# Kernel tuning notes

Measured on AMD Instinct MI355X. Metric: run time of the kernel, lower is better.

The kernel has to match this reference:

```python
import jax, jax.numpy as jnp
import numpy as np

N_ATOMS = 20000        # nodes
N_EDGES = 400000       # avg degree 20
C = 4                  # num_pseudo_species channels
F_IN = 128             # ps_input_size
CONV = [64, 64]        # conv_sizes
HID = [64, 32]         # hidden_sizes
OUT = 1                # output_size (energy)
N_STRUCT = 32          # structures in batch
AVG_ATOMS = 20.0       # average_number_of_atoms
NEG_SLOPE = 0.2        # GAT leaky_relu slope


def setup_inputs() -> dict:
    key = jax.random.key(0)
    ks = jax.random.split(key, 16)
    x = jax.random.normal(ks[0], (N_ATOMS, C, F_IN), dtype=jnp.float32)
    edge_index = jax.random.randint(ks[1], (2, N_EDGES), 0, N_ATOMS)
    batch_ids = jnp.sort(jax.random.randint(ks[2], (N_ATOMS,), 0, N_STRUCT))

    def w(k, shape, fan_in):
        return jax.random.normal(k, shape, dtype=jnp.float32) / np.float32(np.sqrt(fan_in))

    return {
        "x": x,
        "edge_index": edge_index,
        "batch_ids": batch_ids,
        "gamma": jnp.ones((F_IN,), jnp.float32),
        "beta": jnp.zeros((F_IN,), jnp.float32),
        # MultiChannelGATConv 1: F_IN -> 64
        "Wc1": w(ks[3], (C, F_IN, CONV[0]), F_IN),
        "asrc1": w(ks[4], (C, CONV[0]), CONV[0]),
        "adst1": w(ks[5], (C, CONV[0]), CONV[0]),
        # MultiChannelGATConv 2: 64 -> 64
        "Wc2": w(ks[6], (C, CONV[0], CONV[1]), CONV[0]),
        "asrc2": w(ks[7], (C, CONV[1]), CONV[1]),
        "adst2": w(ks[8], (C, CONV[1]), CONV[1]),
        # MultiChannelLinear MLP: 64 -> 64 -> 32
        "Wn1": w(ks[9], (C, CONV[1], HID[0]), CONV[1]),
        "Wn2": w(ks[10], (C, HID[0], HID[1]), HID[0]),
        # out_linear: 32 -> 1
        "Wout": w(ks[11], (C, HID[1], OUT), HID[1]),
    }


def _layer_norm(x, gamma, beta):
    mu = jnp.mean(x, axis=-1, keepdims=True)
    var = jnp.mean((x - mu) ** 2, axis=-1, keepdims=True)
    return (x - mu) * jax.lax.rsqrt(var + 1e-5) * gamma + beta


def _gat_conv(x, W, a_src, a_dst, src, dst):
    # per-channel GATConv (single head, no bias): x [N,C,Fin] -> [N,C,Fout]
    h = jnp.einsum('ncf,cfo->nco', x, W)                       # [N,C,Fout]
    e_src = jnp.einsum('nco,co->nc', h, a_src)                 # [N,C]
    e_dst = jnp.einsum('nco,co->nc', h, a_dst)                 # [N,C]
    logit = jax.nn.leaky_relu(e_src[src] + e_dst[dst], NEG_SLOPE)  # [E,C]
    m = jax.ops.segment_max(logit, dst, num_segments=N_ATOMS)      # [N,C]
    ex = jnp.exp(logit - m[dst])                                   # [E,C]
    den = jax.ops.segment_sum(ex, dst, num_segments=N_ATOMS)       # [N,C]
    alpha = ex / (den[dst] + 1e-16)                                # [E,C]
    msg = alpha[:, :, None] * h[src]                               # [E,C,Fout]
    return jax.ops.segment_sum(msg, dst, num_segments=N_ATOMS)     # [N,C,Fout]


def reference(x, edge_index, batch_ids, gamma, beta,
              Wc1, asrc1, adst1, Wc2, asrc2, adst2,
              Wn1, Wn2, Wout):
    src, dst = edge_index[0], edge_index[1]
    h = _layer_norm(x, gamma, beta)
    h = jax.nn.silu(_gat_conv(h, Wc1, asrc1, adst1, src, dst))
    h = jax.nn.silu(_gat_conv(h, Wc2, asrc2, adst2, src, dst))
    h = jax.nn.silu(jnp.einsum('ncf,cfo->nco', h, Wn1))
    h = jax.nn.silu(jnp.einsum('ncf,cfo->nco', h, Wn2))
    h = jnp.einsum('ncf,cfo->nco', h, Wout)                    # [N,C,1]
    feats = jnp.sum(h, axis=1)                                  # sum_over_components -> [N,1]
    energies = jax.ops.segment_sum(feats, batch_ids, num_segments=N_STRUCT)  # [S,1]
    energies = energies / jnp.sqrt(jnp.float32(C))
    energies = energies / jnp.float32(AVG_ATOMS)
    return energies
```

## Files before the change

### kernel.cpp

```cpp
#include <hip/hip_runtime.h>
#include <hip/hip_bf16.h>
#include <hip/hip_fp16.h>

#define N_ATOMS 20000
#define N_EDGES 400000
#define NCH 4
#define F_IN 128
#define S_OUT 32

__device__ __forceinline__ float silu_f(float v) { return v / (1.f + __expf(-v)); }

typedef _Float16 half8v __attribute__((ext_vector_type(8)));
typedef float f32x4v __attribute__((ext_vector_type(4)));

__device__ __forceinline__ half8v ld_frag(const __half* p) {
    union { float4 f; half8v h; } u;
    u.f = *(const float4*)p;
    return u.h;
}

__device__ __forceinline__ int wave_iscan(int v, int l) {
#pragma unroll
    for (int off = 1; off < 64; off <<= 1) {
        int t = __shfl_up(v, off);
        if (l >= off) v += t;
    }
    return v;
}

__global__ void fill_kernel(float* __restrict__ p, int n, float v) {
    int i = blockIdx.x * blockDim.x + threadIdx.x;
    int stride = gridDim.x * blockDim.x;
    for (; i < n; i += stride) p[i] = v;
}

__global__ void hist_kernel(const int* __restrict__ ei, int* __restrict__ cnt, int E) {
    int e = blockIdx.x * 256 + threadIdx.x;
    if (e < E) atomicAdd(&cnt[ei[E + e]], 1);
}

__global__ __launch_bounds__(256) void scan_l1_kernel(const int* __restrict__ cnt,
                                                      int* __restrict__ rowp,
                                                      int* __restrict__ bsum, int n) {
    int i = blockIdx.x * 256 + threadIdx.x;
    int l = threadIdx.x & 63, w = threadIdx.x >> 6;
    int v = (i < n) ? cnt[i] : 0;
    int incl = wave_iscan(v, l);
    __shared__ int wsum[4];
    if (l == 63) wsum[w] = incl;
    __syncthreads();
    int add = 0;
#pragma unroll
    for (int j = 0; j < 4; ++j) add += (j < w) ? wsum[j] : 0;
    if (i < n) rowp[i] = add + incl - v;
    if (threadIdx.x == 255) bsum[blockIdx.x] = add + incl;
}

__global__ __launch_bounds__(256) void scan_l2_kernel(const int* __restrict__ bsum,
                                                      int* __restrict__ boff,
                                                      int* __restrict__ rowp_n, int nb,
                                                      float* __restrict__ out_zero) {
    int i = threadIdx.x;
    if (i < S_OUT) out_zero[i] = 0.f;
    int l = i & 63, w = i >> 6;
    int v = (i < nb) ? bsum[i] : 0;
    int incl = wave_iscan(v, l);
    __shared__ int wsum[4];
    if (l == 63) wsum[w] = incl;
    __syncthreads();
    int add = 0;
#pragma unroll
    for (int j = 0; j < 4; ++j) add += (j < w) ? wsum[j] : 0;
    if (i < nb) boff[i] = add + incl - v;
    if (i == nb - 1) *rowp_n = add + incl;
}

__global__ __launch_bounds__(256) void scan_l3_kernel(int* __restrict__ rowp,
                                                      const int* __restrict__ boff, int n) {
    int i = blockIdx.x * 256 + threadIdx.x;
    if (i < n) rowp[i] += boff[blockIdx.x];
}

__global__ void scatter_kernel(const int* __restrict__ ei, const int* __restrict__ rowp,
                               int* __restrict__ fill, int* __restrict__ csr_src, int E) {
    int e = blockIdx.x * 256 + threadIdx.x;
    if (e < E) {
        int d = ei[E + e];
        int pos = rowp[d] + atomicAdd(&fill[d], 1);
        csr_src[pos] = ei[e];
    }
}

template <int FIN, int IN_STRIDE, bool IN_HALF, bool IN_CMAJ, bool LN, bool ATT,
          bool SILU_OUT, bool OUT_HALF, bool OUT_CMAJ>
__global__ __launch_bounds__(256) void proj_kernel(const void* __restrict__ inv,
                                                   const float* __restrict__ gamma,
                                                   const float* __restrict__ beta,
                                                   const float* __restrict__ W,
                                                   const float* __restrict__ a_src,
                                                   const float* __restrict__ a_dst,
                                                   void* __restrict__ outv,
                                                   float* __restrict__ es,
                                                   float* __restrict__ ed) {
    constexpr int OCT = FIN / 8;
    constexpr int OM = OCT - 1;
    constexpr int WSH = FIN + 8;
    __shared__ __half Wt[64 * WSH];
    __shared__ __half inl[64 * WSH];
    const int tid = threadIdx.x;
    const int c = blockIdx.y;
    const int n0 = blockIdx.x * 64;
    const int w = tid >> 6;
    const int l = tid & 63;
    const int col = l & 15;
    const int g = l >> 4;

    const float* __restrict__ Wc = W + c * (FIN * 64);
    for (int i = tid; i < (FIN / 2) * 64; i += 256) {
        int kp = i >> 6, oo = i & 63;
        int k = kp * 2;
        float w0 = Wc[(size_t)k * 64 + oo];
        float w1 = Wc[(size_t)(k + 1) * 64 + oo];
        int pos = ((((k >> 3) ^ (oo >> 2)) & OM) << 3) | (k & 7);
        *(__half2*)(&Wt[oo * WSH + pos]) = __floats2half2_rn(w0, w1);
    }
    if (IN_HALF) {
        const __half* __restrict__ inh = (const __half*)inv;
        for (int i = tid; i < 64 * (FIN / 8); i += 256) {
            int nl = i / (FIN / 8), ch = i % (FIN / 8);
            int node = min(n0 + nl, N_ATOMS - 1);
            const __half* src = IN_CMAJ
                ? inh + ((size_t)c * N_ATOMS + node) * 64 + ch * 8
                : inh + (size_t)node * IN_STRIDE + c * FIN + ch * 8;
            *(float4*)(inl + nl * WSH + ch * 8) = *(const float4*)src;
        }
    } else {
        const float* __restrict__ inf = (const float*)inv;
        for (int i = tid; i < 64 * (FIN / 8); i += 256) {
            int nl = i / (FIN / 8), ch = i % (FIN / 8);
            int node = min(n0 + nl, N_ATOMS - 1);
            const float* src = inf + (size_t)node * IN_STRIDE + c * FIN + ch * 8;
            float4 a = *(const float4*)src;
            float4 b = *(const float4*)(src + 4);
            float4 st;
            __half2* sp = (__half2*)&st;
            sp[0] = __floats2half2_rn(a.x, a.y);
            sp[1] = __floats2half2_rn(a.z, a.w);
            sp[2] = __floats2half2_rn(b.x, b.y);
            sp[3] = __floats2half2_rn(b.z, b.w);
            *(float4*)(inl + nl * WSH + ch * 8) = st;
        }
    }
    __syncthreads();

    if (LN) {
        int sub = l >> 4;
        int l16 = l & 15;
        float gv[8], bv8[8];
#pragma unroll
        for (int j = 0; j < 8; ++j) {
            gv[j] = gamma[l16 * 8 + j];
            bv8[j] = beta[l16 * 8 + j];
        }
#pragma unroll
        for (int it = 0; it < 4; ++it) {
            int row = w * 16 + it * 4 + sub;
            __half* rp = inl + row * WSH + l16 * 8;
            float4 raw = *(const float4*)rp;
            __half2* hp = (__half2*)&raw;
            float v[8];
#pragma unroll
            for (int j = 0; j < 4; ++j) {
                float2 f = __half22float2(hp[j]);
                v[2 * j] = f.x;
                v[2 * j + 1] = f.y;
            }
            float s = 0.f, sq = 0.f;
#pragma unroll
            for (int j = 0; j < 8; ++j) { s += v[j]; sq += v[j] * v[j]; }
#pragma unroll
            for (int off = 1; off < 16; off <<= 1) {
                s += __shfl_xor(s, off);
                sq += __shfl_xor(sq, off);
            }
            float mu = s * (1.f / 128.f);
            float rs = rsqrtf(sq * (1.f / 128.f) - mu * mu + 1e-5f);
            float4 st;
            __half2* sp = (__half2*)&st;
#pragma unroll
            for (int j = 0; j < 4; ++j)
                sp[j] = __floats2half2_rn((v[2 * j] - mu) * rs * gv[2 * j] + bv8[2 * j],
                                          (v[2 * j + 1] - mu) * rs * gv[2 * j + 1] + bv8[2 * j + 1]);
            *(float4*)rp = st;
        }
        __syncthreads();
    }

    f32x4v acc[4];
#pragma unroll
    for (int t = 0; t < 4; ++t) acc[t] = (f32x4v){0.f, 0.f, 0.f, 0.f};

    const __half* arow = inl + (w * 16 + col) * WSH + g * 8;
#pragma unroll
    for (int it = 0; it < FIN / 32; ++it) {
        half8v af = ld_frag(arow + it * 32);
        int J = it * 4 + g;
#pragma unroll
        for (int t = 0; t < 4; ++t) {
            int oo = 16 * t + col;
            half8v bf = ld_frag(Wt + oo * WSH + (((J ^ (oo >> 2)) & OM) << 3));
            acc[t] = __builtin_amdgcn_mfma_f32_16x16x32_f16(af, bf, acc[t], 0, 0, 0);
        }
    }

    float av[4], bv[4];
    if (ATT) {
#pragma unroll
        for (int t = 0; t < 4; ++t) {
            av[t] = a_src[c * 64 + 16 * t + col];
            bv[t] = a_dst[c * 64 + 16 * t + col];
        }
    }
#pragma unroll
    for (int r = 0; r < 4; ++r) {
        int node = n0 + w * 16 + g * 4 + r;
        bool valid = node < N_ATOMS;
        if (valid) {
#pragma unroll
            for (int t = 0; t < 4; ++t) {
                float o = acc[t][r];
                if (SILU_OUT) o = silu_f(o);
                size_t idx = OUT_CMAJ ? ((size_t)c * N_ATOMS + node) * 64 + 16 * t + col
                                      : (size_t)node * 256 + c * 64 + 16 * t + col;
                if (OUT_HALF)
                    ((__half*)outv)[idx] = __float2half(o);
                else
                    ((float*)outv)[idx] = o;
            }
        }
        if (ATT) {
            float ps = 0.f, pd = 0.f;
#pragma unroll
            for (int t = 0; t < 4; ++t) {
                ps = fmaf(acc[t][r], av[t], ps);
                pd = fmaf(acc[t][r], bv[t], pd);
            }
#pragma unroll
            for (int off = 1; off < 16; off <<= 1) {
                ps += __shfl_xor(ps, off);
                pd += __shfl_xor(pd, off);
            }
            if (col == 0 && valid) { es[node * NCH + c] = ps; ed[node * NCH + c] = pd; }
        }
    }
}

__global__ __launch_bounds__(256) void gat_gather_kernel(const int* __restrict__ rowp,
                                                         const int* __restrict__ csr_src,
                                                         const float* __restrict__ es,
                                                         const float* __restrict__ ed,
                                                         const __half* __restrict__ h,
                                                         __half* __restrict__ out) {
    int l = threadIdx.x & 63;
    int d = blockIdx.x * 4 + (threadIdx.x >> 6);
    int c = blockIdx.y;
    int q = l & 15;
    int g = l >> 4;
    int grp = l & 48;
    const __half* __restrict__ hc = h + (size_t)c * N_ATOMS * 64;
    int r0 = rowp[d], r1 = rowp[d + 1];
    float edc = ed[d * NCH + c];
    float m = -1e30f, den = 0.f;
    float a0 = 0.f, a1 = 0.f, a2 = 0.f, a3 = 0.f;

    for (int base = r0; base < r1; base += 16) {
        int len = min(16, r1 - base);
        float logit = -1e30f;
        int s = 0;
        if (q < len) {
            s = csr_src[base + q];
            float v = es[s * NCH + c] + edc;
            logit = v >= 0.f ? v : 0.2f * v;
        }
        float cm = logit;
#pragma unroll
        for (int off = 8; off; off >>= 1) cm = fmaxf(cm, __shfl_xor(cm, off));
        float nm = fmaxf(m, cm);
        float resc = __expf(m - nm);
        float ex = (q < len) ? __expf(logit - nm) : 0.f;
        float cs = ex;
#pragma unroll
        for (int off = 8; off; off >>= 1) cs += __shfl_xor(cs, off);
        den = den * resc + cs;
        a0 *= resc; a1 *= resc; a2 *= resc; a3 *= resc;
        m = nm;
#pragma unroll
        for (int j = 0; j < 4; ++j) {
            int e = g + 4 * j;
            bool act = e < len;
            int ee = act ? e : 0;
            float xe = __shfl(ex, grp | ee);
            int se = __shfl(s, grp | ee);
            xe = act ? xe : 0.f;
            float2 hv = *(const float2*)(hc + (size_t)se * 64 + q * 4);
            __half2* hp = (__half2*)&hv;
            float2 f0 = __half22float2(hp[0]), f1 = __half22float2(hp[1]);
            a0 = fmaf(xe, f0.x, a0);
            a1 = fmaf(xe, f0.y, a1);
            a2 = fmaf(xe, f1.x, a2);
            a3 = fmaf(xe, f1.y, a3);
        }
    }
#pragma unroll
    for (int off = 16; off < 64; off <<= 1) {
        a0 += __shfl_xor(a0, off);
        a1 += __shfl_xor(a1, off);
        a2 += __shfl_xor(a2, off);
        a3 += __shfl_xor(a3, off);
    }
    if (g == 0) {
        float inv = 1.f / (den + 1e-16f);
        float2 st;
        __half2* sp = (__half2*)&st;
        sp[0] = __floats2half2_rn(silu_f(a0 * inv), silu_f(a1 * inv));
        sp[1] = __floats2half2_rn(silu_f(a2 * inv), silu_f(a3 * inv));
        *(float2*)(out + ((size_t)c * N_ATOMS + d) * 64 + q * 4) = st;
    }
}

__global__ __launch_bounds__(256) void mlp_fused_kernel(const __half* __restrict__ in,
                                                        const float* __restrict__ W1,
                                                        const float* __restrict__ W2,
                                                        const float* __restrict__ W3,
                                                        const int* __restrict__ bat,
                                                        float* __restrict__ out) {
    constexpr int WSH = 72;
    __shared__ __half W1t[64 * WSH];
    __shared__ __half inl[64 * WSH];
    __shared__ __half t1l[64 * WSH];
    __shared__ __half W2t[NCH][32 * WSH];
    __shared__ float w3l[NCH * 32];
    __shared__ float ynode[64];
    const int tid = threadIdx.x;
    const int n0 = blockIdx.x * 64;
    const int w = tid >> 6;
    const int l = tid & 63;
    const int col = l & 15;
    const int g = l >> 4;

    for (int i = tid; i < NCH * 32 * 32; i += 256) {
        int cc = i >> 10, rem = i & 1023;
        int kp = rem >> 5, o2 = rem & 31;
        int k = kp * 2;
        float a = W2[cc * 2048 + k * 32 + o2];
        float b = W2[cc * 2048 + (k + 1) * 32 + o2];
        int pos = ((((k >> 3) ^ (o2 >> 2)) & 7) << 3) | (k & 7);
        *(__half2*)(&W2t[cc][o2 * WSH + pos]) = __floats2half2_rn(a, b);
    }
    if (tid < NCH * 32) w3l[tid] = W3[tid];

    float yacc[4] = {0.f, 0.f, 0.f, 0.f};

    for (int c = 0; c < NCH; ++c) {
        __syncthreads();
        for (int i = tid; i < 32 * 64; i += 256) {
            int kp = i >> 6, oo = i & 63;
            int k = kp * 2;
            float a = W1[c * 4096 + k * 64 + oo];
            float b = W1[c * 4096 + (k + 1) * 64 + oo];
            int pos = ((((k >> 3) ^ (oo >> 2)) & 7) << 3) | (k & 7);
            *(__half2*)(&W1t[oo * WSH + pos]) = __floats2half2_rn(a, b);
        }
        for (int i = tid; i < 64 * 8; i += 256) {
            int nl = i >> 3, ch = i & 7;
            int node = min(n0 + nl, N_ATOMS - 1);
            *(float4*)(inl + nl * WSH + ch * 8) =
                *(const float4*)(in + ((size_t)c * N_ATOMS + node) * 64 + ch * 8);
        }
        __syncthreads();

        f32x4v acc[4];
#pragma unroll
        for (int t = 0; t < 4; ++t) acc[t] = (f32x4v){0.f, 0.f, 0.f, 0.f};
        const __half* arow = inl + (w * 16 + col) * WSH + g * 8;
#pragma unroll
        for (int it = 0; it < 2; ++it) {
            half8v af = ld_frag(arow + it * 32);
            int J = it * 4 + g;
#pragma unroll
            for (int t = 0; t < 4; ++t) {
                int oo = 16 * t + col;
                half8v bf = ld_frag(W1t + oo * WSH + (((J ^ (oo >> 2)) & 7) << 3));
                acc[t] = __builtin_amdgcn_mfma_f32_16x16x32_f16(af, bf, acc[t], 0, 0, 0);
            }
        }
#pragma unroll
        for (int t = 0; t < 4; ++t)
#pragma unroll
            for (int r = 0; r < 4; ++r)
                t1l[(w * 16 + g * 4 + r) * WSH + 16 * t + col] = __float2half(silu_f(acc[t][r]));

        f32x4v acc2[2];
        acc2[0] = (f32x4v){0.f, 0.f, 0.f, 0.f};
        acc2[1] = (f32x4v){0.f, 0.f, 0.f, 0.f};
        const __half* arow2 = t1l + (w * 16 + col) * WSH + g * 8;
#pragma unroll
        for (int it = 0; it < 2; ++it) {
            half8v af = ld_frag(arow2 + it * 32);
            int J = it * 4 + g;
#pragma unroll
            for (int t = 0; t < 2; ++t) {
                int o2 = 16 * t + col;
                half8v bf = ld_frag(&W2t[c][o2 * WSH + (((J ^ (o2 >> 2)) & 7) << 3)]);
                acc2[t] = __builtin_amdgcn_mfma_f32_16x16x32_f16(af, bf, acc2[t], 0, 0, 0);
            }
        }
        float w3a = w3l[c * 32 + col], w3b = w3l[c * 32 + 16 + col];
#pragma unroll
        for (int r = 0; r < 4; ++r) {
            float p = silu_f(acc2[0][r]) * w3a + silu_f(acc2[1][r]) * w3b;
#pragma unroll
            for (int off = 1; off < 16; off <<= 1) p += __shfl_xor(p, off);
            yacc[r] += p;
        }
    }

    if (col == 0) {
#pragma unroll
        for (int r = 0; r < 4; ++r) ynode[w * 16 + g * 4 + r] = yacc[r];
    }
    __syncthreads();
    if (tid < 64) {
        int node = n0 + tid;
        bool act = node < N_ATOMS;
        float val = act ? ynode[tid] * 0.025f : 0.f;
        int b = act ? bat[min(node, N_ATOMS - 1)] : 0;
        unsigned long long rem = __ballot(act);
        while (rem) {
            int lead = (int)__ffsll(rem) - 1;
            int bl = __shfl(b, lead);
            bool mine = act && (b == bl);
            float t = mine ? val : 0.f;
#pragma unroll
            for (int off = 32; off; off >>= 1) t += __shfl_xor(t, off);
            if (tid == lead) atomicAdd(out + bl, t);
            rem &= ~__ballot(mine);
        }
    }
}

extern "C" void kernel_launch(void* const* d_in, const int* in_sizes, int n_in,
                              void* d_out, int out_size, void* d_ws, size_t ws_size,
                              hipStream_t stream) {
    const float* x     = (const float*)d_in[0];
    const int*   ei    = (const int*)d_in[1];
    const int*   bat   = (const int*)d_in[2];
    const float* gamma = (const float*)d_in[3];
    const float* beta  = (const float*)d_in[4];
    const float* Wc1   = (const float*)d_in[5];
    const float* as1   = (const float*)d_in[6];
    const float* ad1   = (const float*)d_in[7];
    const float* Wc2   = (const float*)d_in[8];
    const float* as2   = (const float*)d_in[9];
    const float* ad2   = (const float*)d_in[10];
    const float* Wn1   = (const float*)d_in[11];
    const float* Wn2   = (const float*)d_in[12];
    const float* Wout  = (const float*)d_in[13];
    float* out = (float*)d_out;

    float* A    = (float*)d_ws;
    float* B    = A + 10240000;
    float* es   = B + 5120000;
    float* ed   = es + 80000;
    int* rowp   = (int*)(ed + 80000);
    int* cnt    = rowp + 20004;
    int* fillc  = cnt + 20000;
    int* csr    = fillc + 20000;
    int* bsum   = csr + 400000;
    int* boff   = bsum + 128;
    __half* C1h = (__half*)A;
    __half* C2h = (__half*)(A + 2560000);
    __half* Bh  = (__half*)B;

    dim3 blk(256);
    const int NB = (N_ATOMS + 255) / 256;
    const int NT64 = (N_ATOMS + 63) / 64;

    fill_kernel<<<80, blk, 0, stream>>>((float*)cnt, 40000, 0.f);
    hist_kernel<<<(N_EDGES + 255) / 256, blk, 0, stream>>>(ei, cnt, N_EDGES);
    scan_l1_kernel<<<NB, blk, 0, stream>>>(cnt, rowp, bsum, N_ATOMS);
    scan_l2_kernel<<<1, blk, 0, stream>>>(bsum, boff, rowp + N_ATOMS, NB, out);
    scan_l3_kernel<<<NB, blk, 0, stream>>>(rowp, boff, N_ATOMS);
    scatter_kernel<<<(N_EDGES + 255) / 256, blk, 0, stream>>>(ei, rowp, fillc, csr, N_EDGES);

    proj_kernel<128, NCH * F_IN, false, false, true, true, false, true, true>
        <<<dim3(NT64, NCH), blk, 0, stream>>>(x, gamma, beta, Wc1, as1, ad1, Bh, es, ed);
    gat_gather_kernel<<<dim3(N_ATOMS / 4, NCH), blk, 0, stream>>>(rowp, csr, es, ed, Bh, C1h);

    proj_kernel<64, 64, true, true, false, true, false, true, true>
        <<<dim3(NT64, NCH), blk, 0, stream>>>(C1h, gamma, beta, Wc2, as2, ad2, Bh, es, ed);
    gat_gather_kernel<<<dim3(N_ATOMS / 4, NCH), blk, 0, stream>>>(rowp, csr, es, ed, Bh, C2h);

    mlp_fused_kernel<<<NT64, blk, 0, stream>>>(C2h, Wn1, Wn2, Wout, bat, out);
}
```

Baseline: 203.5 us.

## Map one destination node per 16-lane group in GAT gather, channel-major scores

The gather kernel now gives each 16-lane quarter of a wave its own destination node, four nodes per wave, where before a whole wave handled one node. Each quarter processes its own neighbour chunks in lockstep up to the wave's maximum degree, so the cross-group reduction at the end is gone. The edge loop is unrolled to issue four independent row loads at once. Attention scores es/ed are stored channel-major so per-channel reads are contiguous. The lockstep loop can waste lanes when degrees within a wave differ, and it does redundant shuffles over inactive edges.

Measured after the change: 173.6 us. -14.7%, faster.

```diff
diff --git a/kernel.cpp b/kernel.cpp
--- a/kernel.cpp
+++ b/kernel.cpp
@@ -250,7 +250,10 @@
                 ps += __shfl_xor(ps, off);
                 pd += __shfl_xor(pd, off);
             }
-            if (col == 0 && valid) { es[node * NCH + c] = ps; ed[node * NCH + c] = pd; }
+            if (col == 0 && valid) {
+                es[(size_t)c * N_ATOMS + node] = ps;
+                ed[(size_t)c * N_ATOMS + node] = pd;
+            }
         }
     }
 }
@@ -262,24 +265,29 @@
                                                          const __half* __restrict__ h,
                                                          __half* __restrict__ out) {
     int l = threadIdx.x & 63;
-    int d = blockIdx.x * 4 + (threadIdx.x >> 6);
+    int wv = threadIdx.x >> 6;
     int c = blockIdx.y;
-    int q = l & 15;
-    int g = l >> 4;
-    int grp = l & 48;
+    int g = l >> 4, q = l & 15, grp = l & 48;
+    int d = blockIdx.x * 16 + wv * 4 + g;
     const __half* __restrict__ hc = h + (size_t)c * N_ATOMS * 64;
+    const float* __restrict__ esc = es + (size_t)c * N_ATOMS;
     int r0 = rowp[d], r1 = rowp[d + 1];
-    float edc = ed[d * NCH + c];
+    int deg = r1 - r0;
+    float edc = ed[(size_t)c * N_ATOMS + d];
+    int maxdeg = deg;
+#pragma unroll
+    for (int off = 16; off < 64; off <<= 1) maxdeg = max(maxdeg, __shfl_xor(maxdeg, off));
+
     float m = -1e30f, den = 0.f;
     float a0 = 0.f, a1 = 0.f, a2 = 0.f, a3 = 0.f;
 
-    for (int base = r0; base < r1; base += 16) {
-        int len = min(16, r1 - base);
+    for (int bo = 0; bo < maxdeg; bo += 16) {
+        int len = min(16, deg - bo);
         float logit = -1e30f;
         int s = 0;
         if (q < len) {
-            s = csr_src[base + q];
-            float v = es[s * NCH + c] + edc;
+            s = csr_src[r0 + bo + q];
+            float v = esc[s] + edc;
             logit = v >= 0.f ? v : 0.2f * v;
         }
         float cm = logit;
@@ -295,37 +303,35 @@
         a0 *= resc; a1 *= resc; a2 *= resc; a3 *= resc;
         m = nm;
 #pragma unroll
-        for (int j = 0; j < 4; ++j) {
-            int e = g + 4 * j;
-            bool act = e < len;
-            int ee = act ? e : 0;
-            float xe = __shfl(ex, grp | ee);
-            int se = __shfl(s, grp | ee);
-            xe = act ? xe : 0.f;
-            float2 hv = *(const float2*)(hc + (size_t)se * 64 + q * 4);
-            __half2* hp = (__half2*)&hv;
-            float2 f0 = __half22float2(hp[0]), f1 = __half22float2(hp[1]);
-            a0 = fmaf(xe, f0.x, a0);
-            a1 = fmaf(xe, f0.y, a1);
-            a2 = fmaf(xe, f1.x, a2);
-            a3 = fmaf(xe, f1.y, a3);
-        }
-    }
-#pragma unroll
-    for (int off = 16; off < 64; off <<= 1) {
-        a0 += __shfl_xor(a0, off);
-        a1 += __shfl_xor(a1, off);
-        a2 += __shfl_xor(a2, off);
-        a3 += __shfl_xor(a3, off);
-    }
-    if (g == 0) {
-        float inv = 1.f / (den + 1e-16f);
-        float2 st;
-        __half2* sp = (__half2*)&st;
-        sp[0] = __floats2half2_rn(silu_f(a0 * inv), silu_f(a1 * inv));
-        sp[1] = __floats2half2_rn(silu_f(a2 * inv), silu_f(a3 * inv));
-        *(float2*)(out + ((size_t)c * N_ATOMS + d) * 64 + q * 4) = st;
-    }
+        for (int e = 0; e < 16; e += 4) {
+            int s0 = __shfl(s, grp | e),       s1 = __shfl(s, grp | (e + 1));
+            int s2 = __shfl(s, grp | (e + 2)), s3 = __shfl(s, grp | (e + 3));
+            float x0 = __shfl(ex, grp | e),       x1 = __shfl(ex, grp | (e + 1));
+            float x2 = __shfl(ex, grp | (e + 2)), x3 = __shfl(ex, grp | (e + 3));
+            float2 hv0 = *(const float2*)(hc + (size_t)s0 * 64 + q * 4);
+            float2 hv1 = *(const float2*)(hc + (size_t)s1 * 64 + q * 4);
+            float2 hv2 = *(const float2*)(hc + (size_t)s2 * 64 + q * 4);
+            float2 hv3 = *(const float2*)(hc + (size_t)s3 * 64 + q * 4);
+            __half2* p0 = (__half2*)&hv0;
+            __half2* p1 = (__half2*)&hv1;
+            __half2* p2 = (__half2*)&hv2;
+            __half2* p3 = (__half2*)&hv3;
+            float2 f00 = __half22float2(p0[0]), f01 = __half22float2(p0[1]);
+            float2 f10 = __half22float2(p1[0]), f11 = __half22float2(p1[1]);
+            float2 f20 = __half22float2(p2[0]), f21 = __half22float2(p2[1]);
+            float2 f30 = __half22float2(p3[0]), f31 = __half22float2(p3[1]);
+            a0 = fmaf(x0, f00.x, fmaf(x1, f10.x, fmaf(x2, f20.x, fmaf(x3, f30.x, a0))));
+            a1 = fmaf(x0, f00.y, fmaf(x1, f10.y, fmaf(x2, f20.y, fmaf(x3, f30.y, a1))));
+            a2 = fmaf(x0, f01.x, fmaf(x1, f11.x, fmaf(x2, f21.x, fmaf(x3, f31.x, a2))));
+            a3 = fmaf(x0, f01.y, fmaf(x1, f11.y, fmaf(x2, f21.y, fmaf(x3, f31.y, a3))));
+        }
+    }
+    float inv = 1.f / (den + 1e-16f);
+    float2 st;
+    __half2* sp = (__half2*)&st;
+    sp[0] = __floats2half2_rn(silu_f(a0 * inv), silu_f(a1 * inv));
+    sp[1] = __floats2half2_rn(silu_f(a2 * inv), silu_f(a3 * inv));
+    *(float2*)(out + ((size_t)c * N_ATOMS + d) * 64 + q * 4) = st;
 }
 
 __global__ __launch_bounds__(256) void mlp_fused_kernel(const __half* __restrict__ in,
@@ -495,11 +501,11 @@
 
     proj_kernel<128, NCH * F_IN, false, false, true, true, false, true, true>
         <<<dim3(NT64, NCH), blk, 0, stream>>>(x, gamma, beta, Wc1, as1, ad1, Bh, es, ed);
-    gat_gather_kernel<<<dim3(N_ATOMS / 4, NCH), blk, 0, stream>>>(rowp, csr, es, ed, Bh, C1h);
+    gat_gather_kernel<<<dim3(N_ATOMS / 16, NCH), blk, 0, stream>>>(rowp, csr, es, ed, Bh, C1h);
 
     proj_kernel<64, 64, true, true, false, true, false, true, true>
         <<<dim3(NT64, NCH), blk, 0, stream>>>(C1h, gamma, beta, Wc2, as2, ad2, Bh, es, ed);
-    gat_gather_kernel<<<dim3(N_ATOMS / 4, NCH), blk, 0, stream>>>(rowp, csr, es, ed, Bh, C2h);
+    gat_gather_kernel<<<dim3(N_ATOMS / 16, NCH), blk, 0, stream>>>(rowp, csr, es, ed, Bh, C2h);
 
     mlp_fused_kernel<<<NT64, blk, 0, stream>>>(C2h, Wn1, Wn2, Wout, bat, out);
 }
```
